# Performance work log

Hardware: AMD Instinct MI355X
Metric: run time of the kernel (lower is better)

The kernel has to match this reference:

```python
import jax, jax.numpy as jnp
import numpy as np

H = 10  # hidden_size


def _lstm_cell(x, h, c, Wih, Whh, bih, bhh):
    # PyTorch LSTMCell: gates ordered i, f, g, o
    gates = x @ Wih.T + bih + h @ Whh.T + bhh  # [B, 4H]
    i, f, g, o = jnp.split(gates, 4, axis=-1)
    c_new = jax.nn.sigmoid(f) * c + jax.nn.sigmoid(i) * jnp.tanh(g)
    h_new = jax.nn.sigmoid(o) * jnp.tanh(c_new)
    return h_new, c_new


def setup_inputs() -> dict:
    key = jax.random.key(0)
    ks = jax.random.split(key, 12)
    B, T = 16384, 2048
    s = 1.0 / np.sqrt(H)  # PyTorch LSTMCell init scale
    inp = {
        "x": jax.random.normal(ks[0], (B, T, 2), dtype=jnp.float32),
        "WihA": jax.random.uniform(ks[1], (4 * H, 2), minval=-s, maxval=s),
        "WhhA": jax.random.uniform(ks[2], (4 * H, H), minval=-s, maxval=s),
        "bihA": jax.random.uniform(ks[3], (4 * H,), minval=-s, maxval=s),
        "bhhA": jax.random.uniform(ks[4], (4 * H,), minval=-s, maxval=s),
        "WihB": jax.random.uniform(ks[5], (4 * H, 1), minval=-s, maxval=s),
        "WhhB": jax.random.uniform(ks[6], (4 * H, H), minval=-s, maxval=s),
        "bihB": jax.random.uniform(ks[7], (4 * H,), minval=-s, maxval=s),
        "bhhB": jax.random.uniform(ks[8], (4 * H,), minval=-s, maxval=s),
        "Wlin": jax.random.uniform(ks[9], (1, H), minval=-s, maxval=s),
        "blin": jax.random.uniform(ks[10], (1,), minval=-s, maxval=s),
    }
    return inp


def reference(x, WihA, WhhA, bihA, bhhA, WihB, WhhB, bihB, bhhB, Wlin, blin):
    B, T, _ = x.shape
    # time-major pairs: step 2k uses cellB on x[:, 2k, :1], step 2k+1 uses cellA on x[:, 2k+1, :]
    xs = jnp.transpose(x, (1, 0, 2)).reshape(T // 2, 2, B, 2)  # [T/2, 2, B, 2]
    h0 = jnp.zeros((B, H), dtype=x.dtype)
    c0 = jnp.zeros((B, H), dtype=x.dtype)

    def step(carry, x_pair):
        h, c = carry
        h, c = _lstm_cell(x_pair[0][:, :1], h, c, WihB, WhhB, bihB, bhhB)
        h, c = _lstm_cell(x_pair[1], h, c, WihA, WhhA, bihA, bhhA)
        return (h, c), None

    (h, c), _ = jax.lax.scan(step, (h0, c0), xs)
    # original stacks all hx but only uses the last timestep
    return jax.nn.sigmoid(h @ Wlin.T + blin)  # [B, 1]
```

## Files before the change

### kernel.cpp

```cpp
#include <hip/hip_runtime.h>
#include <math.h>

#define H 10
#define BATCH 16384
#define NPAIRS 1024
#define EPW 6
#define GSTRIDE 12

#define LOG2E 1.44269504088896340736f

#if __has_builtin(__builtin_amdgcn_exp2f)
#define EXP2(x) __builtin_amdgcn_exp2f(x)
#else
#define EXP2(x) exp2f(x)
#endif

__device__ __forceinline__ float fast_rcp(float x) { return __builtin_amdgcn_rcpf(x); }

__global__ void __launch_bounds__(64, 2)
lstm_kernel(const float* __restrict__ x,
            const float* __restrict__ WihA, const float* __restrict__ WhhA,
            const float* __restrict__ bihA, const float* __restrict__ bhhA,
            const float* __restrict__ WihB, const float* __restrict__ WhhB,
            const float* __restrict__ bihB, const float* __restrict__ bhhB,
            const float* __restrict__ Wlin, const float* __restrict__ blin,
            float* __restrict__ out)
{
    const int lane    = threadIdx.x;
    const int e_local = lane / H;
    const int j       = lane - e_local * H;
    const bool active = lane < EPW * H;
    const int elem    = blockIdx.x * EPW + e_local;
    const bool valid  = active && (elem < BATCH);
    const int jj      = active ? j : 0;
    const int elem_c  = valid ? elem : 0;

    __shared__ __align__(16) float hbuf[84];
    const int waddr = active ? (e_local * GSTRIDE + j) : (72 + (lane - 60));
    const int rbase = e_local * GSTRIDE;

    float wA[4][H], wB[4][H];
    float bA[4], bB[4], wxA0[4], wxA1[4], wxB[4];
#pragma unroll
    for (int g = 0; g < 4; ++g) {
        const float s = (g == 2) ? (2.0f * LOG2E) : (-LOG2E);
        const int row = g * H + jj;
        bA[g]   = s * (bihA[row] + bhhA[row]);
        bB[g]   = s * (bihB[row] + bhhB[row]);
        wxA0[g] = s * WihA[row * 2 + 0];
        wxA1[g] = s * WihA[row * 2 + 1];
        wxB[g]  = s * WihB[row];
#pragma unroll
        for (int k = 0; k < H; ++k) {
            wA[g][k] = s * WhhA[row * H + k];
            wB[g][k] = s * WhhB[row * H + k];
        }
    }
#pragma unroll
    for (int g = 0; g < 4; ++g) {
        asm volatile("" : "+v"(bA[g]), "+v"(bB[g]), "+v"(wxA0[g]),
                          "+v"(wxA1[g]), "+v"(wxB[g]));
#pragma unroll
        for (int k = 0; k < H; ++k) {
            asm volatile("" : "+v"(wA[g][k]), "+v"(wB[g][k]));
        }
    }

    const float4* __restrict__ xr = (const float4*)x + (size_t)elem_c * NPAIRS;

    float h = 0.0f, c = 0.0f;
    float4 xp = xr[0];

#pragma unroll 2
    for (int p = 0; p < NPAIRS; ++p) {
        const int pn = (p + 1 < NPAIRS) ? (p + 1) : p;
        const float4 xnext = xr[pn];

        {
            hbuf[waddr] = h;
            float y0 = fmaf(wxB[0], xp.x, bB[0]);
            float y1 = fmaf(wxB[1], xp.x, bB[1]);
            float y2 = fmaf(wxB[2], xp.x, bB[2]);
            float y3 = fmaf(wxB[3], xp.x, bB[3]);
            const float4 ha = *reinterpret_cast<const float4*>(&hbuf[rbase]);
            const float4 hb = *reinterpret_cast<const float4*>(&hbuf[rbase + 4]);
            const float2 hc = *reinterpret_cast<const float2*>(&hbuf[rbase + 8]);
            float hh[H] = {ha.x, ha.y, ha.z, ha.w, hb.x, hb.y, hb.z, hb.w,
                           hc.x, hc.y};
#pragma unroll
            for (int k = 0; k < H; ++k) {
                y0 = fmaf(wB[0][k], hh[k], y0);
                y1 = fmaf(wB[1][k], hh[k], y1);
                y2 = fmaf(wB[2][k], hh[k], y2);
                y3 = fmaf(wB[3][k], hh[k], y3);
            }
            const float ef = EXP2(y1);
            const float ei = EXP2(y0);
            const float eg = EXP2(-__builtin_fabsf(y2));
            const float sf = fast_rcp(1.0f + ef);
            const float d1 = (1.0f + ei) * (1.0f + eg);
            const float it = __builtin_copysignf((1.0f - eg) * fast_rcp(d1), y2);
            const float cn = fmaf(sf, c, it);
            const float eo = EXP2(y3);
            const float ec = EXP2((-2.0f * LOG2E) * __builtin_fabsf(cn));
            const float d2 = (1.0f + eo) * (1.0f + ec);
            h = __builtin_copysignf((1.0f - ec) * fast_rcp(d2), cn);
            c = cn;
        }

        {
            hbuf[waddr] = h;
            float y0 = fmaf(wxA1[0], xp.w, fmaf(wxA0[0], xp.z, bA[0]));
            float y1 = fmaf(wxA1[1], xp.w, fmaf(wxA0[1], xp.z, bA[1]));
            float y2 = fmaf(wxA1[2], xp.w, fmaf(wxA0[2], xp.z, bA[2]));
            float y3 = fmaf(wxA1[3], xp.w, fmaf(wxA0[3], xp.z, bA[3]));
            const float4 ha = *reinterpret_cast<const float4*>(&hbuf[rbase]);
            const float4 hb = *reinterpret_cast<const float4*>(&hbuf[rbase + 4]);
            const float2 hc = *reinterpret_cast<const float2*>(&hbuf[rbase + 8]);
            float hh[H] = {ha.x, ha.y, ha.z, ha.w, hb.x, hb.y, hb.z, hb.w,
                           hc.x, hc.y};
#pragma unroll
            for (int k = 0; k < H; ++k) {
                y0 = fmaf(wA[0][k], hh[k], y0);
                y1 = fmaf(wA[1][k], hh[k], y1);
                y2 = fmaf(wA[2][k], hh[k], y2);
                y3 = fmaf(wA[3][k], hh[k], y3);
            }
            const float ef = EXP2(y1);
            const float ei = EXP2(y0);
            const float eg = EXP2(-__builtin_fabsf(y2));
            const float sf = fast_rcp(1.0f + ef);
            const float d1 = (1.0f + ei) * (1.0f + eg);
            const float it = __builtin_copysignf((1.0f - eg) * fast_rcp(d1), y2);
            const float cn = fmaf(sf, c, it);
            const float eo = EXP2(y3);
            const float ec = EXP2((-2.0f * LOG2E) * __builtin_fabsf(cn));
            const float d2 = (1.0f + eo) * (1.0f + ec);
            h = __builtin_copysignf((1.0f - ec) * fast_rcp(d2), cn);
            c = cn;
        }

        xp = xnext;
    }

    {
        const float v = Wlin[jj] * h;
        hbuf[waddr] = v;
        const float4 ha = *reinterpret_cast<const float4*>(&hbuf[rbase]);
        const float4 hb = *reinterpret_cast<const float4*>(&hbuf[rbase + 4]);
        const float2 hc = *reinterpret_cast<const float2*>(&hbuf[rbase + 8]);
        const float s = ((ha.x + ha.y) + (ha.z + ha.w)) +
                        ((hb.x + hb.y) + (hb.z + hb.w)) + (hc.x + hc.y);
        if (valid && j == 0) {
            const float y = s + blin[0];
            out[elem] = fast_rcp(1.0f + EXP2(-LOG2E * y));
        }
    }
}

extern "C" void kernel_launch(void* const* d_in, const int* in_sizes, int n_in,
                              void* d_out, int out_size, void* d_ws, size_t ws_size,
                              hipStream_t stream) {
    const float* x    = (const float*)d_in[0];
    const float* WihA = (const float*)d_in[1];
    const float* WhhA = (const float*)d_in[2];
    const float* bihA = (const float*)d_in[3];
    const float* bhhA = (const float*)d_in[4];
    const float* WihB = (const float*)d_in[5];
    const float* WhhB = (const float*)d_in[6];
    const float* bihB = (const float*)d_in[7];
    const float* bhhB = (const float*)d_in[8];
    const float* Wlin = (const float*)d_in[9];
    const float* blin = (const float*)d_in[10];
    float* out = (float*)d_out;

    const int grid = (BATCH + EPW - 1) / EPW;
    hipLaunchKernelGGL(lstm_kernel, dim3(grid), dim3(64), 0, stream,
                       x, WihA, WhhA, bihA, bhhA, WihB, WhhB, bihB, bhhB,
                       Wlin, blin, out);
}
```

Baseline: 1.163 ms.

## Use packed FP32 FMAs for recurrent matvec and merge gate reciprocals

Replaces the per-lane 40 scalar FMAs of the hidden-state matvec with 20 v_pk_mul/v_pk_fma operations on paired weights, followed by a horizontal add per gate. It also rewrites the cell-state update to use a single reciprocal over the combined denominator instead of two, and changes occupancy hints to waves_per_eu(2,3). The aim is to shorten the serial per-step dependency chain and cut VALU issue count. In exchange it adds reduction adds, risks overflow or inf in the product of denominators for large gate values, and changes rounding order.

```diff
diff --git a/kernel.cpp b/kernel.cpp
--- a/kernel.cpp
+++ b/kernel.cpp
@@ -15,9 +15,22 @@
 #define EXP2(x) exp2f(x)
 #endif
 
+typedef float v2f __attribute__((ext_vector_type(2)));
+
 __device__ __forceinline__ float fast_rcp(float x) { return __builtin_amdgcn_rcpf(x); }
 
-__global__ void __launch_bounds__(64, 2)
+__device__ __forceinline__ v2f pk_mul(v2f a, v2f b) {
+    v2f d;
+    asm("v_pk_mul_f32 %0, %1, %2" : "=v"(d) : "v"(a), "v"(b));
+    return d;
+}
+__device__ __forceinline__ v2f pk_fma(v2f a, v2f b, v2f c) {
+    v2f d;
+    asm("v_pk_fma_f32 %0, %1, %2, %3" : "=v"(d) : "v"(a), "v"(b), "v"(c));
+    return d;
+}
+
+__global__ void __launch_bounds__(64) __attribute__((amdgpu_waves_per_eu(2, 3)))
 lstm_kernel(const float* __restrict__ x,
             const float* __restrict__ WihA, const float* __restrict__ WhhA,
             const float* __restrict__ bihA, const float* __restrict__ bhhA,
@@ -39,7 +52,7 @@
     const int waddr = active ? (e_local * GSTRIDE + j) : (72 + (lane - 60));
     const int rbase = e_local * GSTRIDE;
 
-    float wA[4][H], wB[4][H];
+    v2f wA2[4][5], wB2[4][5];
     float bA[4], bB[4], wxA0[4], wxA1[4], wxB[4];
 #pragma unroll
     for (int g = 0; g < 4; ++g) {
@@ -51,9 +64,9 @@
         wxA1[g] = s * WihA[row * 2 + 1];
         wxB[g]  = s * WihB[row];
 #pragma unroll
-        for (int k = 0; k < H; ++k) {
-            wA[g][k] = s * WhhA[row * H + k];
-            wB[g][k] = s * WhhB[row * H + k];
+        for (int m = 0; m < 5; ++m) {
+            wA2[g][m] = (v2f){s * WhhA[row * H + 2 * m], s * WhhA[row * H + 2 * m + 1]};
+            wB2[g][m] = (v2f){s * WhhB[row * H + 2 * m], s * WhhB[row * H + 2 * m + 1]};
         }
     }
 #pragma unroll
@@ -61,8 +74,8 @@
         asm volatile("" : "+v"(bA[g]), "+v"(bB[g]), "+v"(wxA0[g]),
                           "+v"(wxA1[g]), "+v"(wxB[g]));
 #pragma unroll
-        for (int k = 0; k < H; ++k) {
-            asm volatile("" : "+v"(wA[g][k]), "+v"(wB[g][k]));
+        for (int m = 0; m < 5; ++m) {
+            asm volatile("" : "+v"(wA2[g][m]), "+v"(wB2[g][m]));
         }
     }
 
@@ -78,30 +91,44 @@
 
         {
             hbuf[waddr] = h;
-            float y0 = fmaf(wxB[0], xp.x, bB[0]);
-            float y1 = fmaf(wxB[1], xp.x, bB[1]);
-            float y2 = fmaf(wxB[2], xp.x, bB[2]);
-            float y3 = fmaf(wxB[3], xp.x, bB[3]);
+            const float b0 = fmaf(wxB[0], xp.x, bB[0]);
+            const float b1 = fmaf(wxB[1], xp.x, bB[1]);
+            const float b2 = fmaf(wxB[2], xp.x, bB[2]);
+            const float b3 = fmaf(wxB[3], xp.x, bB[3]);
             const float4 ha = *reinterpret_cast<const float4*>(&hbuf[rbase]);
             const float4 hb = *reinterpret_cast<const float4*>(&hbuf[rbase + 4]);
             const float2 hc = *reinterpret_cast<const float2*>(&hbuf[rbase + 8]);
-            float hh[H] = {ha.x, ha.y, ha.z, ha.w, hb.x, hb.y, hb.z, hb.w,
-                           hc.x, hc.y};
-#pragma unroll
-            for (int k = 0; k < H; ++k) {
-                y0 = fmaf(wB[0][k], hh[k], y0);
-                y1 = fmaf(wB[1][k], hh[k], y1);
-                y2 = fmaf(wB[2][k], hh[k], y2);
-                y3 = fmaf(wB[3][k], hh[k], y3);
-            }
+            const v2f h01 = (v2f){ha.x, ha.y}, h23 = (v2f){ha.z, ha.w};
+            const v2f h45 = (v2f){hb.x, hb.y}, h67 = (v2f){hb.z, hb.w};
+            const v2f h89 = (v2f){hc.x, hc.y};
+
+            v2f a0 = pk_mul(wB2[0][0], h01);
+            v2f a1 = pk_mul(wB2[1][0], h01);
+            v2f a2 = pk_mul(wB2[2][0], h01);
+            v2f a3 = pk_mul(wB2[3][0], h01);
+            a0 = pk_fma(wB2[0][1], h23, a0); a1 = pk_fma(wB2[1][1], h23, a1);
+            a2 = pk_fma(wB2[2][1], h23, a2); a3 = pk_fma(wB2[3][1], h23, a3);
+            a0 = pk_fma(wB2[0][2], h45, a0); a1 = pk_fma(wB2[1][2], h45, a1);
+            a2 = pk_fma(wB2[2][2], h45, a2); a3 = pk_fma(wB2[3][2], h45, a3);
+            a0 = pk_fma(wB2[0][3], h67, a0); a1 = pk_fma(wB2[1][3], h67, a1);
+            a2 = pk_fma(wB2[2][3], h67, a2); a3 = pk_fma(wB2[3][3], h67, a3);
+            a0 = pk_fma(wB2[0][4], h89, a0); a1 = pk_fma(wB2[1][4], h89, a1);
+            a2 = pk_fma(wB2[2][4], h89, a2); a3 = pk_fma(wB2[3][4], h89, a3);
+
+            const float y0 = (a0.x + a0.y) + b0;
+            const float y1 = (a1.x + a1.y) + b1;
+            const float y2 = (a2.x + a2.y) + b2;
+            const float y3 = (a3.x + a3.y) + b3;
+
             const float ef = EXP2(y1);
             const float ei = EXP2(y0);
             const float eg = EXP2(-__builtin_fabsf(y2));
-            const float sf = fast_rcp(1.0f + ef);
+            const float eo = EXP2(y3);
+            const float opf = 1.0f + ef;
             const float d1 = (1.0f + ei) * (1.0f + eg);
-            const float it = __builtin_copysignf((1.0f - eg) * fast_rcp(d1), y2);
-            const float cn = fmaf(sf, c, it);
-            const float eo = EXP2(y3);
+            const float tg = __builtin_copysignf((1.0f - eg) * opf, y2);
+            const float num = fmaf(c, d1, tg);
+            const float cn = num * fast_rcp(opf * d1);
             const float ec = EXP2((-2.0f * LOG2E) * __builtin_fabsf(cn));
             const float d2 = (1.0f + eo) * (1.0f + ec);
             h = __builtin_copysignf((1.0f - ec) * fast_rcp(d2), cn);
@@ -110,30 +137,44 @@
 
         {
             hbuf[waddr] = h;
-            float y0 = fmaf(wxA1[0], xp.w, fmaf(wxA0[0], xp.z, bA[0]));
-            float y1 = fmaf(wxA1[1], xp.w, fmaf(wxA0[1], xp.z, bA[1]));
-            float y2 = fmaf(wxA1[2], xp.w, fmaf(wxA0[2], xp.z, bA[2]));
-            float y3 = fmaf(wxA1[3], xp.w, fmaf(wxA0[3], xp.z, bA[3]));
+            const float b0 = fmaf(wxA1[0], xp.w, fmaf(wxA0[0], xp.z, bA[0]));
+            const float b1 = fmaf(wxA1[1], xp.w, fmaf(wxA0[1], xp.z, bA[1]));
+            const float b2 = fmaf(wxA1[2], xp.w, fmaf(wxA0[2], xp.z, bA[2]));
+            const float b3 = fmaf(wxA1[3], xp.w, fmaf(wxA0[3], xp.z, bA[3]));
             const float4 ha = *reinterpret_cast<const float4*>(&hbuf[rbase]);
             const float4 hb = *reinterpret_cast<const float4*>(&hbuf[rbase + 4]);
             const float2 hc = *reinterpret_cast<const float2*>(&hbuf[rbase + 8]);
-            float hh[H] = {ha.x, ha.y, ha.z, ha.w, hb.x, hb.y, hb.z, hb.w,
-                           hc.x, hc.y};
-#pragma unroll
-            for (int k = 0; k < H; ++k) {
-                y0 = fmaf(wA[0][k], hh[k], y0);
-                y1 = fmaf(wA[1][k], hh[k], y1);
-                y2 = fmaf(wA[2][k], hh[k], y2);
-                y3 = fmaf(wA[3][k], hh[k], y3);
-            }
+            const v2f h01 = (v2f){ha.x, ha.y}, h23 = (v2f){ha.z, ha.w};
+            const v2f h45 = (v2f){hb.x, hb.y}, h67 = (v2f){hb.z, hb.w};
+            const v2f h89 = (v2f){hc.x, hc.y};
+
+            v2f a0 = pk_mul(wA2[0][0], h01);
+            v2f a1 = pk_mul(wA2[1][0], h01);
+            v2f a2 = pk_mul(wA2[2][0], h01);
+            v2f a3 = pk_mul(wA2[3][0], h01);
+            a0 = pk_fma(wA2[0][1], h23, a0); a1 = pk_fma(wA2[1][1], h23, a1);
+            a2 = pk_fma(wA2[2][1], h23, a2); a3 = pk_fma(wA2[3][1], h23, a3);
+            a0 = pk_fma(wA2[0][2], h45, a0); a1 = pk_fma(wA2[1][2], h45, a1);
+            a2 = pk_fma(wA2[2][2], h45, a2); a3 = pk_fma(wA2[3][2], h45, a3);
+            a0 = pk_fma(wA2[0][3], h67, a0); a1 = pk_fma(wA2[1][3], h67, a1);
+            a2 = pk_fma(wA2[2][3], h67, a2); a3 = pk_fma(wA2[3][3], h67, a3);
+            a0 = pk_fma(wA2[0][4], h89, a0); a1 = pk_fma(wA2[1][4], h89, a1);
+            a2 = pk_fma(wA2[2][4], h89, a2); a3 = pk_fma(wA2[3][4], h89, a3);
+
+            const float y0 = (a0.x + a0.y) + b0;
+            const float y1 = (a1.x + a1.y) + b1;
+            const float y2 = (a2.x + a2.y) + b2;
+            const float y3 = (a3.x + a3.y) + b3;
+
             const float ef = EXP2(y1);
             const float ei = EXP2(y0);
             const float eg = EXP2(-__builtin_fabsf(y2));
-            const float sf = fast_rcp(1.0f + ef);
+            const float eo = EXP2(y3);
+            const float opf = 1.0f + ef;
             const float d1 = (1.0f + ei) * (1.0f + eg);
-            const float it = __builtin_copysignf((1.0f - eg) * fast_rcp(d1), y2);
-            const float cn = fmaf(sf, c, it);
-            const float eo = EXP2(y3);
+            const float tg = __builtin_copysignf((1.0f - eg) * opf, y2);
+            const float num = fmaf(c, d1, tg);
+            const float cn = num * fast_rcp(opf * d1);
             const float ec = EXP2((-2.0f * LOG2E) * __builtin_fabsf(cn));
             const float d2 = (1.0f + eo) * (1.0f + ec);
             h = __builtin_copysignf((1.0f - ec) * fast_rcp(d2), cn);
```

Result: no change. 1.164 ms (+0.1%).
